# Kernel tuning notes

Measured on AMD Instinct MI355X. Metric: run time of the kernel, lower is better.

The kernel has to match this reference:

```python
import jax, jax.numpy as jnp
import numpy as np

B, L, V, D, C, R = 8, 2048, 32000, 512, 64, 64
NBLK = 2           # n_layers - 1
H = 2 * D          # stem hidden dim
STD = 0.02


def _ln(x, w, b):
    m = x.mean(-1, keepdims=True)
    v = ((x - m) ** 2).mean(-1, keepdims=True)
    return (x - m) / jnp.sqrt(v + 1e-5) * w + b


def setup_inputs() -> dict:
    key = jax.random.key(0)
    ks = jax.random.split(key, 16)
    n = lambda k, shp: jax.random.normal(k, shp, dtype=jnp.float32) * STD
    return {
        "token_ids": jax.random.randint(ks[0], (B, L), 0, V),
        "tok_emb": n(ks[1], (V, D)),
        "pos_emb": n(ks[2], (L, D)),
        "stem_ln_w": jnp.ones((NBLK, D), jnp.float32),
        "stem_ln_b": jnp.zeros((NBLK, D), jnp.float32),
        "stem_w1": n(ks[3], (NBLK, D, H)),
        "stem_b1": jnp.zeros((NBLK, H), jnp.float32),
        "stem_w2": n(ks[4], (NBLK, H, D)),
        "stem_b2": jnp.zeros((NBLK, D), jnp.float32),
        "role_ln_w": jnp.ones((D,), jnp.float32),
        "role_ln_b": jnp.zeros((D,), jnp.float32),
        "Wa": n(ks[5], (D, R)),
        "Wb": n(ks[6], (D, R)),
        "Wc": n(ks[7], (D, R)),
        "class_a": n(ks[8], (C, R)),
        "class_b": n(ks[9], (C, R)),
        "class_c": n(ks[10], (C, R)),
        "query_ln_w": jnp.ones((D,), jnp.float32),
        "query_ln_b": jnp.zeros((D,), jnp.float32),
        "Wq": n(ks[11], (D, C)),
        "bq": jnp.zeros((C,), jnp.float32),
    }


def reference(token_ids, tok_emb, pos_emb, stem_ln_w, stem_ln_b, stem_w1,
              stem_b1, stem_w2, stem_b2, role_ln_w, role_ln_b, Wa, Wb, Wc,
              class_a, class_b, class_c, query_ln_w, query_ln_b, Wq, bq):
    seq_len = token_ids.shape[1]
    x = tok_emb[token_ids] + pos_emb[:seq_len][None, :, :]  # [B,L,D]
    for i in range(NBLK):
        h = _ln(x, stem_ln_w[i], stem_ln_b[i])
        h = jax.nn.gelu(h @ stem_w1[i] + stem_b1[i], approximate=False)
        x = x + h @ stem_w2[i] + stem_b2[i]
    prefix = _ln(x[:, :-1], role_ln_w, role_ln_b)  # [B,L-1,D]
    a = jnp.tanh(prefix @ Wa)
    b = jnp.tanh(prefix @ Wb)
    c = jnp.tanh(prefix @ Wc)
    ua = jnp.einsum('blr,cr->blc', a, class_a)  # [B,L-1,C]
    ub = jnp.einsum('blr,cr->blc', b, class_b)
    uc = jnp.einsum('blr,cr->blc', c, class_c)
    # exact ordered-triplet sum  sum_{i<j<k} ua_i * ub_j * uc_k  via exclusive cumsums
    prefA = jnp.cumsum(ua, axis=1) - ua            # sum_{i<j} ua_i
    t = ub * prefA
    prefT = jnp.cumsum(t, axis=1) - t              # sum_{j<k} ub_j * prefA_j
    s = (uc * prefT).sum(axis=1)                   # [B,C]
    Lp = max(seq_len - 1, 1)
    denom = max(Lp * (Lp - 1) * (Lp - 2) / 6.0, 1.0)
    q = _ln(x[:, -1], query_ln_w, query_ln_b)
    return s / denom + q @ Wq + bq
```

## Files before the change

### kernel.cpp

```cpp
#include <hip/hip_runtime.h>

#define NROWS 16384
#define LSEQ  2048
#define NB    8

typedef short v8s __attribute__((ext_vector_type(8)));
typedef float v4f __attribute__((ext_vector_type(4)));

__device__ __forceinline__ unsigned short f2bf(float f) {
    unsigned int u = __float_as_uint(f);
    return (unsigned short)((u + 0x7fffu + ((u >> 16) & 1u)) >> 16);
}
__device__ __forceinline__ float bf2f(unsigned short u) {
    return __uint_as_float(((unsigned int)u) << 16);
}

__device__ __forceinline__ void glds16(const void* g, void* l) {
    __builtin_amdgcn_global_load_lds(
        (__attribute__((address_space(1))) void*)g,
        (__attribute__((address_space(3))) void*)l,
        16, 0, 0);
}

__device__ __forceinline__ float fast_gelu(float v) {
    float z = fabsf(v) * 0.70710678118654752f;
    float t = __builtin_amdgcn_rcpf(1.0f + 0.3275911f * z);
    float poly = t * (0.254829592f + t * (-0.284496736f + t * (1.421413741f +
                 t * (-1.453152027f + t * 1.061405429f))));
    float erfz = 1.0f - poly * __expf(-z * z);
    float er = copysignf(erfz, v);
    return 0.5f * v * (1.0f + er);
}
__device__ __forceinline__ float fast_tanh(float y) {
    float e = __expf(2.0f * y);
    return (e - 1.0f) * __builtin_amdgcn_rcpf(e + 1.0f);
}

__device__ __forceinline__ long swizzled_row(int b, int wave) {
    int T = (b & 7) + (((b >> 3) & 15) << 3);
    int chunk = b >> 7;
    return (long)T * 128 + chunk * 4 + wave;
}

__global__ __launch_bounds__(256) void setup_kernel(
        const int* __restrict__ ids,
        const float* __restrict__ tok, const float* __restrict__ pos,
        const float* __restrict__ g0, const float* __restrict__ b0,
        const float* __restrict__ rolew, const float* __restrict__ roleb,
        const float* __restrict__ b1all,
        unsigned short* __restrict__ x, float* __restrict__ rowstat0,
        const float* __restrict__ w1, const float* __restrict__ w2,
        const float* __restrict__ wa, const float* __restrict__ wb, const float* __restrict__ wc,
        const float* __restrict__ ca, const float* __restrict__ cb, const float* __restrict__ cc,
        unsigned short* __restrict__ w1T, unsigned short* __restrict__ w2T,
        unsigned short* __restrict__ wabcT, unsigned short* __restrict__ clsb,
        float* __restrict__ c1buf, float* __restrict__ c2buf,
        float* __restrict__ c1a, float* __restrict__ c2a) {
    int blk = blockIdx.x;
    int t = threadIdx.x;
    if (blk < 4096) {
        int wave = t >> 6, lane = t & 63;
        long row = swizzled_row(blk, wave);
        int l = (int)(row & (LSEQ - 1));
        int id = ids[row];
        int d = lane * 8;
        float4 t0 = *(const float4*)(tok + (size_t)id * 512 + d);
        float4 t1 = *(const float4*)(tok + (size_t)id * 512 + d + 4);
        float4 p0 = *(const float4*)(pos + (size_t)l * 512 + d);
        float4 p1 = *(const float4*)(pos + (size_t)l * 512 + d + 4);
        float a[8] = {t0.x + p0.x, t0.y + p0.y, t0.z + p0.z, t0.w + p0.w,
                      t1.x + p1.x, t1.y + p1.y, t1.z + p1.z, t1.w + p1.w};
        unsigned int xp[4];
        #pragma unroll
        for (int i = 0; i < 4; ++i)
            xp[i] = (unsigned int)f2bf(a[2 * i]) | ((unsigned int)f2bf(a[2 * i + 1]) << 16);
        *(uint4*)(x + row * 512 + d) = *(uint4*)xp;
        float s = 0.f, s2 = 0.f;
        #pragma unroll
        for (int i = 0; i < 8; ++i) { s += a[i]; s2 += a[i] * a[i]; }
        #pragma unroll
        for (int o = 32; o > 0; o >>= 1) { s += __shfl_down(s, o); s2 += __shfl_down(s2, o); }
        if (lane == 0) {
            rowstat0[row * 2] = s;
            rowstat0[row * 2 + 1] = s2;
        }
    } else if (blk < 6240) {
        int id = blk - 4096;
        int tx = t & 31, ty = t >> 5;
        const float* in; unsigned short* out; int R, C, bx, by, ldo;
        const float* gfold = nullptr;
        if (id < 1024) {
            int l = id >> 9, r = id & 511;
            in = w1 + l * 524288; out = w1T + l * 524288;
            R = 512; C = 1024; bx = r & 31; by = r >> 5; ldo = 512;
            gfold = g0 + l * 512;
        } else if (id < 2048) {
            int l = (id - 1024) >> 9, r = (id - 1024) & 511;
            in = w2 + l * 524288; out = w2T + l * 524288;
            R = 1024; C = 512; bx = r & 15; by = r >> 4; ldo = 1024;
        } else {
            int g = (id - 2048) >> 5, r = (id - 2048) & 31;
            in = (g == 0) ? wa : (g == 1) ? wb : wc;
            out = wabcT + g * 32768;
            R = 512; C = 64; bx = r & 1; by = r >> 1; ldo = 512;
            gfold = rolew;
        }
        __shared__ unsigned short tile[32][33];
        int c0 = bx * 32, r0 = by * 32;
        for (int i = ty; i < 32; i += 8) {
            int r = r0 + i, c = c0 + tx;
            float v = (r < R && c < C) ? in[(size_t)r * C + c] : 0.f;
            if (gfold && r < R) v *= gfold[r];
            tile[i][tx] = f2bf(v);
        }
        __syncthreads();
        for (int i = ty; i < 32; i += 8) {
            int c = c0 + i, r = r0 + tx;
            if (r < R && c < C) out[(size_t)c * ldo + r] = tile[tx][i];
        }
    } else if (blk < 6243) {
        int g = blk - 6240;
        const float* src = (g == 0) ? ca : (g == 1) ? cb : cc;
        unsigned short* dst = clsb + g * 4096;
        for (int i = t; i < 4096; i += 256) dst[i] = f2bf(src[i]);
    } else if (blk < 6251) {
        int c = blk - 6243;
        int l = c >> 2, nb = c & 3;
        int n = nb * 256 + t;
        const float* W = w1 + l * 524288;
        const float* g = g0 + l * 512;
        const float* b = b0 + l * 512;
        float a1 = 0.f, a2 = 0.f;
        for (int k = 0; k < 512; ++k) {
            float w = W[(size_t)k * 1024 + n];
            a1 += g[k] * w;
            a2 += b[k] * w;
        }
        c1buf[l * 1024 + n] = a1;
        c2buf[l * 1024 + n] = a2 + b1all[l * 1024 + n];
    } else {
        if (t < 192) {
            int gi = t >> 6, r = t & 63;
            const float* W = (gi == 0) ? wa : (gi == 1) ? wb : wc;
            float a1 = 0.f, a2 = 0.f;
            for (int k = 0; k < 512; ++k) {
                float w = W[(size_t)k * 64 + r];
                a1 += rolew[k] * w;
                a2 += roleb[k] * w;
            }
            c1a[t] = a1;
            c2a[t] = a2;
        }
    }
}

template <int SM>
__global__ __launch_bounds__(512, 1) void gemm_w1(
        const unsigned short* __restrict__ A,
        const unsigned short* __restrict__ BT,
        const float* __restrict__ c1, const float* __restrict__ c2,
        const float* __restrict__ stats,
        unsigned short* __restrict__ Cout) {
    constexpr int BN = 256, NFC = 4, FCH = 2, NLB = 2, BH = 128;
    constexpr int lda = 512, ldb = 512, ldc = 1024, K = 512;
    __shared__ unsigned short Ab[2][2][128 * 64] __attribute__((aligned(16)));
    __shared__ unsigned short Bb[2][2][BH * 64] __attribute__((aligned(16)));
    const int t = threadIdx.x;
    const int lane = t & 63, w = t >> 6;
    const int quad = lane >> 4, l16 = lane & 15;
    const int wmh = w >> 2;
    const int wn  = w & 3;
    const int bhalf = wn >> 1, bbase = (wn & 1) * (BN / 4);
    const long tileM = (long)blockIdx.x * 256;
    const long tileN = (long)blockIdx.y * BN;

    const int rl = lane >> 3;
    const int cl = ((lane & 7) ^ rl) * 8;

    const unsigned short* pa[2][2];
    #pragma unroll
    for (int h = 0; h < 2; ++h)
        #pragma unroll
        for (int q = 0; q < 2; ++q)
            pa[h][q] = A + (tileM + h * 128 + w * 16 + q * 8 + rl) * (size_t)lda + cl;
    const unsigned short* pb[2][2];
    #pragma unroll
    for (int h = 0; h < 2; ++h)
        #pragma unroll
        for (int q = 0; q < 2; ++q)
            pb[h][q] = BT + (tileN + h * BH + w * 16 + q * 8 + rl) * (size_t)ldb + cl;
    int kA = 0, kB = 0;

    auto stageA = [&](int buf, int h) {
        glds16(pa[h][0] + kA, &Ab[buf][h][(w * 2 + 0) * 512]);
        glds16(pa[h][1] + kA, &Ab[buf][h][(w * 2 + 1) * 512]);
    };
    auto stageB = [&](int buf, int h) {
        glds16(pb[h][0] + kB, &Bb[buf][h][(w * 2 + 0) * 512]);
        glds16(pb[h][1] + kB, &Bb[buf][h][(w * 2 + 1) * 512]);
    };

    const int xl = l16 & 7;
    const int ak0 = l16 * 64 + (((quad    ) ^ xl) * 8);
    const int ak1 = l16 * 64 + (((quad + 4) ^ xl) * 8);

    stageA(0, 0); stageA(0, 1); kA = 64;
    stageB(0, 0); stageB(0, 1); kB = 64;
    stageB(1, 0); stageB(1, 1); kB = 128;

    v4f acc[8][NFC] = {};
    const int nt = K >> 6;

    asm volatile("s_waitcnt vmcnt(%0)" :: "i"(2 * NLB) : "memory");
    __builtin_amdgcn_s_barrier();

    for (int tt = 0; tt < nt; ++tt) {
        const int bi = tt & 1;
        const unsigned short* Ah = &Ab[bi][wmh][0];
        const unsigned short* Bh = &Bb[bi][bhalf][bbase * 64];
        v8s af[4][2], bf[NFC][2];

        #pragma unroll
        for (int fr = 0; fr < 4; ++fr) {
            af[fr][0] = *(const v8s*)(Ah + fr * 1024 + ak0);
            af[fr][1] = *(const v8s*)(Ah + fr * 1024 + ak1);
        }
        #pragma unroll
        for (int fc = 0; fc < FCH; ++fc) {
            bf[fc][0] = *(const v8s*)(Bh + fc * 1024 + ak0);
            bf[fc][1] = *(const v8s*)(Bh + fc * 1024 + ak1);
        }
        if (tt + 1 < nt) stageA(bi ^ 1, 0);
        __builtin_amdgcn_s_barrier();
        asm volatile("s_waitcnt lgkmcnt(0)" ::: "memory");
        __builtin_amdgcn_s_setprio(1);
        #pragma unroll
        for (int fr = 0; fr < 4; ++fr)
            #pragma unroll
            for (int fc = 0; fc < FCH; ++fc) {
                acc[fr][fc] = __builtin_amdgcn_mfma_f32_16x16x32_bf16(bf[fc][0], af[fr][0], acc[fr][fc], 0, 0, 0);
                acc[fr][fc] = __builtin_amdgcn_mfma_f32_16x16x32_bf16(bf[fc][1], af[fr][1], acc[fr][fc], 0, 0, 0);
            }
        __builtin_amdgcn_s_setprio(0);
        __builtin_amdgcn_s_barrier();

        #pragma unroll
        for (int fc = FCH; fc < NFC; ++fc) {
            bf[fc][0] = *(const v8s*)(Bh + fc * 1024 + ak0);
            bf[fc][1] = *(const v8s*)(Bh + fc * 1024 + ak1);
        }
        if (tt + 1 < nt) stageA(bi ^ 1, 1);
        kA += 64;
        __builtin_amdgcn_s_barrier();
        asm volatile("s_waitcnt lgkmcnt(0)" ::: "memory");
        __builtin_amdgcn_s_setprio(1);
        #pragma unroll
        for (int fr = 0; fr < 4; ++fr)
            #pragma unroll
            for (int fc = FCH; fc < NFC; ++fc) {
                acc[fr][fc] = __builtin_amdgcn_mfma_f32_16x16x32_bf16(bf[fc][0], af[fr][0], acc[fr][fc], 0, 0, 0);
                acc[fr][fc] = __builtin_amdgcn_mfma_f32_16x16x32_bf16(bf[fc][1], af[fr][1], acc[fr][fc], 0, 0, 0);
            }
        __builtin_amdgcn_s_setprio(0);
        __builtin_amdgcn_s_barrier();

        #pragma unroll
        for (int fr = 0; fr < 4; ++fr) {
            af[fr][0] = *(const v8s*)(Ah + (fr + 4) * 1024 + ak0);
            af[fr][1] = *(const v8s*)(Ah + (fr + 4) * 1024 + ak1);
        }
        if (tt + 2 < nt) stageB(bi, 0);
        __builtin_amdgcn_s_barrier();
        asm volatile("s_waitcnt lgkmcnt(0)" ::: "memory");
        __builtin_amdgcn_s_setprio(1);
        #pragma unroll
        for (int fr = 0; fr < 4; ++fr)
            #pragma unroll
            for (int fc = 0; fc < FCH; ++fc) {
                acc[fr + 4][fc] = __builtin_amdgcn_mfma_f32_16x16x32_bf16(bf[fc][0], af[fr][0], acc[fr + 4][fc], 0, 0, 0);
                acc[fr + 4][fc] = __builtin_amdgcn_mfma_f32_16x16x32_bf16(bf[fc][1], af[fr][1], acc[fr + 4][fc], 0, 0, 0);
            }
        __builtin_amdgcn_s_setprio(0);
        __builtin_amdgcn_s_barrier();

        if (tt + 2 < nt) stageB(bi, 1);
        kB += 64;
        if (tt + 2 < nt)
            asm volatile("s_waitcnt vmcnt(%0)" :: "i"(2 * NLB) : "memory");
        else if (tt + 1 < nt)
            asm volatile("s_waitcnt vmcnt(0)" ::: "memory");
        __builtin_amdgcn_s_barrier();
        __builtin_amdgcn_s_setprio(1);
        #pragma unroll
        for (int fr = 0; fr < 4; ++fr)
            #pragma unroll
            for (int fc = FCH; fc < NFC; ++fc) {
                acc[fr + 4][fc] = __builtin_amdgcn_mfma_f32_16x16x32_bf16(bf[fc][0], af[fr][0], acc[fr + 4][fc], 0, 0, 0);
                acc[fr + 4][fc] = __builtin_amdgcn_mfma_f32_16x16x32_bf16(bf[fc][1], af[fr][1], acc[fr + 4][fc], 0, 0, 0);
            }
        __builtin_amdgcn_s_setprio(0);
        __builtin_amdgcn_s_barrier();
    }

    #pragma unroll
    for (int fr = 0; fr < 8; ++fr) {
        long m = tileM + wmh * 128 + fr * 16 + l16;
        float s1, s2;
        if (SM == 0) {
            float2 st = *(const float2*)&stats[m * 2];
            s1 = st.x; s2 = st.y;
        } else {
            float4 q0 = *(const float4*)&stats[m * 8];
            float4 q1 = *(const float4*)&stats[m * 8 + 4];
            s1 = q0.x + q0.z + q1.x + q1.z;
            s2 = q0.y + q0.w + q1.y + q1.w;
        }
        float mu = s1 * (1.0f / 512.0f);
        float rinv = 1.0f / sqrtf(s2 * (1.0f / 512.0f) - mu * mu + 1e-5f);
        float rmu = rinv * mu;
        #pragma unroll
        for (int fc = 0; fc < NFC; ++fc) {
            long n0 = tileN + wn * (BN / 4) + fc * 16 + quad * 4;
            float4 c14 = *(const float4*)&c1[n0];
            float4 c24 = *(const float4*)&c2[n0];
            const float* c1p = (const float*)&c14;
            const float* c2p = (const float*)&c24;
            unsigned short pk[4];
            #pragma unroll
            for (int r = 0; r < 4; ++r)
                pk[r] = f2bf(fast_gelu(rinv * acc[fr][fc][r] - rmu * c1p[r] + c2p[r]));
            *(ushort4*)&Cout[m * ldc + n0] = *(ushort4*)pk;
        }
    }
}

__global__ __launch_bounds__(512, 1) void gemm_w2(
        const unsigned short* __restrict__ A,
        const unsigned short* __restrict__ BT,
        const float* __restrict__ bias,
        unsigned short* __restrict__ x,
        float* __restrict__ rowpart) {
    constexpr int BN = 128, NFC = 2, FCH = 1, NLB = 1, BH = 64;
    constexpr int lda = 1024, ldb = 1024, K = 1024;
    __shared__ unsigned short Ab[2][2][128 * 64] __attribute__((aligned(16)));
    __shared__ unsigned short Bb[2][2][BH * 64] __attribute__((aligned(16)));
    const int t = threadIdx.x;
    const int lane = t & 63, w = t >> 6;
    const int quad = lane >> 4, l16 = lane & 15;
    const int wmh = w >> 2;
    const int wn  = w & 3;
    const int bhalf = wn >> 1, bbase = (wn & 1) * (BN / 4);
    const long tileM = (long)blockIdx.x * 256;
    const int yb = blockIdx.y;
    const long tileN = (long)yb * BN;

    const int rl = lane >> 3;
    const int cl = ((lane & 7) ^ rl) * 8;

    const unsigned short* pa[2][2];
    #pragma unroll
    for (int h = 0; h < 2; ++h)
        #pragma unroll
        for (int q = 0; q < 2; ++q)
            pa[h][q] = A + (tileM + h * 128 + w * 16 + q * 8 + rl) * (size_t)lda + cl;
    const unsigned short* pb[2];
    #pragma unroll
    for (int h = 0; h < 2; ++h)
        pb[h] = BT + (tileN + h * BH + w * 8 + rl) * (size_t)ldb + cl;
    int kA = 0, kB = 0;

    auto stageA = [&](int buf, int h) {
        glds16(pa[h][0] + kA, &Ab[buf][h][(w * 2 + 0) * 512]);
        glds16(pa[h][1] + kA, &Ab[buf][h][(w * 2 + 1) * 512]);
    };
    auto stageB = [&](int buf, int h) {
        glds16(pb[h] + kB, &Bb[buf][h][w * 512]);
    };

    const int xl = l16 & 7;
    const int ak0 = l16 * 64 + (((quad    ) ^ xl) * 8);
    const int ak1 = l16 * 64 + (((quad + 4) ^ xl) * 8);

    stageA(0, 0); stageA(0, 1); kA = 64;
    stageB(0, 0); stageB(0, 1); kB = 64;
    stageB(1, 0); stageB(1, 1); kB = 128;

    v4f acc[8][NFC] = {};
    const int nt = K >> 6;

    asm volatile("s_waitcnt vmcnt(%0)" :: "i"(2 * NLB) : "memory");
    __builtin_amdgcn_s_barrier();

    for (int tt = 0; tt < nt; ++tt) {
        const int bi = tt & 1;
        const unsigned short* Ah = &Ab[bi][wmh][0];
        const unsigned short* Bh = &Bb[bi][bhalf][bbase * 64];
        v8s af[4][2], bf[NFC][2];

        #pragma unroll
        for (int fr = 0; fr < 4; ++fr) {
            af[fr][0] = *(const v8s*)(Ah + fr * 1024 + ak0);
            af[fr][1] = *(const v8s*)(Ah + fr * 1024 + ak1);
        }
        #pragma unroll
        for (int fc = 0; fc < FCH; ++fc) {
            bf[fc][0] = *(const v8s*)(Bh + fc * 1024 + ak0);
            bf[fc][1] = *(const v8s*)(Bh + fc * 1024 + ak1);
        }
        if (tt + 1 < nt) stageA(bi ^ 1, 0);
        __builtin_amdgcn_s_barrier();
        asm volatile("s_waitcnt lgkmcnt(0)" ::: "memory");
        __builtin_amdgcn_s_setprio(1);
        #pragma unroll
        for (int fr = 0; fr < 4; ++fr)
            #pragma unroll
            for (int fc = 0; fc < FCH; ++fc) {
                acc[fr][fc] = __builtin_amdgcn_mfma_f32_16x16x32_bf16(bf[fc][0], af[fr][0], acc[fr][fc], 0, 0, 0);
                acc[fr][fc] = __builtin_amdgcn_mfma_f32_16x16x32_bf16(bf[fc][1], af[fr][1], acc[fr][fc], 0, 0, 0);
            }
        __builtin_amdgcn_s_setprio(0);
        __builtin_amdgcn_s_barrier();

        #pragma unroll
        for (int fc = FCH; fc < NFC; ++fc) {
            bf[fc][0] = *(const v8s*)(Bh + fc * 1024 + ak0);
            bf[fc][1] = *(const v8s*)(Bh + fc * 1024 + ak1);
        }
        if (tt + 1 < nt) stageA(bi ^ 1, 1);
        kA += 64;
        __builtin_amdgcn_s_barrier();
        asm volatile("s_waitcnt lgkmcnt(0)" ::: "memory");
        __builtin_amdgcn_s_setprio(1);
        #pragma unroll
        for (int fr = 0; fr < 4; ++fr)
            #pragma unroll
            for (int fc = FCH; fc < NFC; ++fc) {
                acc[fr][fc] = __builtin_amdgcn_mfma_f32_16x16x32_bf16(bf[fc][0], af[fr][0], acc[fr][fc], 0, 0, 0);
                acc[fr][fc] = __builtin_amdgcn_mfma_f32_16x16x32_bf16(bf[fc][1], af[fr][1], acc[fr][fc], 0, 0, 0);
            }
        __builtin_amdgcn_s_setprio(0);
        __builtin_amdgcn_s_barrier();

        #pragma unroll
        for (int fr = 0; fr < 4; ++fr) {
            af[fr][0] = *(const v8s*)(Ah + (fr + 4) * 1024 + ak0);
            af[fr][1] = *(const v8s*)(Ah + (fr + 4) * 1024 + ak1);
        }
        if (tt + 2 < nt) stageB(bi, 0);
        __builtin_amdgcn_s_barrier();
        asm volatile("s_waitcnt lgkmcnt(0)" ::: "memory");
        __builtin_amdgcn_s_setprio(1);
        #pragma unroll
        for (int fr = 0; fr < 4; ++fr)
            #pragma unroll
            for (int fc = 0; fc < FCH; ++fc) {
                acc[fr + 4][fc] = __builtin_amdgcn_mfma_f32_16x16x32_bf16(bf[fc][0], af[fr][0], acc[fr + 4][fc], 0, 0, 0);
                acc[fr + 4][fc] = __builtin_amdgcn_mfma_f32_16x16x32_bf16(bf[fc][1], af[fr][1], acc[fr + 4][fc], 0, 0, 0);
            }
        __builtin_amdgcn_s_setprio(0);
        __builtin_amdgcn_s_barrier();

        if (tt + 2 < nt) stageB(bi, 1);
        kB += 64;
        if (tt + 2 < nt)
            asm volatile("s_waitcnt vmcnt(%0)" :: "i"(2 * NLB) : "memory");
        else if (tt + 1 < nt)
            asm volatile("s_waitcnt vmcnt(0)" ::: "memory");
        __builtin_amdgcn_s_barrier();
        __builtin_amdgcn_s_setprio(1);
        #pragma unroll
        for (int fr = 0; fr < 4; ++fr)
            #pragma unroll
            for (int fc = FCH; fc < NFC; ++fc) {
                acc[fr + 4][fc] = __builtin_amdgcn_mfma_f32_16x16x32_bf16(bf[fc][0], af[fr][0], acc[fr + 4][fc], 0, 0, 0);
                acc[fr + 4][fc] = __builtin_amdgcn_mfma_f32_16x16x32_bf16(bf[fc][1], af[fr][1], acc[fr + 4][fc], 0, 0, 0);
            }
        __builtin_amdgcn_s_setprio(0);
        __builtin_amdgcn_s_barrier();
    }

    float p1[8], p2[8];
    #pragma unroll
    for (int fr = 0; fr < 8; ++fr) { p1[fr] = 0.f; p2[fr] = 0.f; }
    #pragma unroll
    for (int fr = 0; fr < 8; ++fr) {
        long m = tileM + wmh * 128 + fr * 16 + l16;
        #pragma unroll
        for (int fc = 0; fc < NFC; ++fc) {
            long n0 = tileN + wn * (BN / 4) + fc * 16 + quad * 4;
            float4 bi4 = *(const float4*)&bias[n0 - tileN + yb * BN];
            const float* bip = (const float*)&bi4;
            ushort4 xr4 = *(const ushort4*)&x[m * 512 + n0];
            const unsigned short* xp = (const unsigned short*)&xr4;
            unsigned short pk[4];
            #pragma unroll
            for (int r = 0; r < 4; ++r) {
                float v = acc[fr][fc][r] + bip[r] + bf2f(xp[r]);
                p1[fr] += v; p2[fr] += v * v;
                pk[r] = f2bf(v);
            }
            *(ushort4*)&x[m * 512 + n0] = *(ushort4*)pk;
        }
    }
    #pragma unroll
    for (int fr = 0; fr < 8; ++fr) {
        p1[fr] += __shfl_xor(p1[fr], 16); p1[fr] += __shfl_xor(p1[fr], 32);
        p2[fr] += __shfl_xor(p2[fr], 16); p2[fr] += __shfl_xor(p2[fr], 32);
    }
    float* red = (float*)&Ab[0][0][0];
    if (quad == 0) {
        #pragma unroll
        for (int fr = 0; fr < 8; ++fr) {
            int r = wmh * 128 + fr * 16 + l16;
            red[r * 4 + wn] = p1[fr];
            red[1024 + r * 4 + wn] = p2[fr];
        }
    }
    __syncthreads();
    if (t < 256) {
        int r = t;
        float s1 = red[r * 4] + red[r * 4 + 1] + red[r * 4 + 2] + red[r * 4 + 3];
        float s2 = red[1024 + r * 4] + red[1024 + r * 4 + 1] + red[1024 + r * 4 + 2] + red[1024 + r * 4 + 3];
        long m = tileM + r;
        rowpart[m * 8 + yb * 2]     = s1;
        rowpart[m * 8 + yb * 2 + 1] = s2;
    }
}

__global__ __launch_bounds__(256) void tanh_class_kernel(
        const unsigned short* __restrict__ A,
        const unsigned short* __restrict__ WT,
        const unsigned short* __restrict__ cls,
        const float* __restrict__ rowpart,
        const float* __restrict__ c1a, const float* __restrict__ c2a,
        unsigned short* __restrict__ uu) {
    __shared__ unsigned short As[128][40] __attribute__((aligned(16)));
    __shared__ unsigned short Bs[64][40] __attribute__((aligned(16)));
    __shared__ unsigned short P[128 * 72] __attribute__((aligned(16)));
    const int t = threadIdx.x;
    const int lane = t & 63, wave = t >> 6;
    const int quad = lane >> 4, l16 = lane & 15;
    const int wm = (wave >> 1) * 64, wn = (wave & 1) * 32;
    const long tileM = (long)blockIdx.x * 128;
    const int g = blockIdx.y;
    const int arow = t >> 2, acol = (t & 3) * 8;

    const unsigned short* BT = WT + g * 32768;
    v8s cf[2][2];
    #pragma unroll
    for (int ks = 0; ks < 2; ++ks)
        #pragma unroll
        for (int j = 0; j < 2; ++j)
            cf[ks][j] = *(const v8s*)&cls[g * 4096 + (wn + j * 16 + l16) * 64 + ks * 32 + quad * 8];

    const unsigned short* gA0 = A + (tileM + arow) * 512 + acol;
    const unsigned short* gA1 = gA0 + 64 * 512;
    const unsigned short* gB0 = BT + arow * 512 + acol;

    v4f acc[4][2] = {};
    uint4 a0, a1, b0;
    a0 = *(const uint4*)gA0; a1 = *(const uint4*)gA1; gA0 += 32; gA1 += 32;
    b0 = *(const uint4*)gB0; gB0 += 32;
    *(uint4*)&As[arow][acol] = a0;
    *(uint4*)&As[arow + 64][acol] = a1;
    *(uint4*)&Bs[arow][acol] = b0;

    for (int kk = 0; kk < 16; ++kk) {
        __syncthreads();
        const bool more = kk < 15;
        if (more) {
            a0 = *(const uint4*)gA0; a1 = *(const uint4*)gA1; gA0 += 32; gA1 += 32;
            b0 = *(const uint4*)gB0; gB0 += 32;
        }
        v8s af[4], bfr[2];
        #pragma unroll
        for (int i = 0; i < 4; ++i) af[i] = *(const v8s*)&As[wm + i * 16 + l16][quad * 8];
        #pragma unroll
        for (int j = 0; j < 2; ++j) bfr[j] = *(const v8s*)&Bs[wn + j * 16 + l16][quad * 8];
        #pragma unroll
        for (int i = 0; i < 4; ++i)
            #pragma unroll
            for (int j = 0; j < 2; ++j)
                acc[i][j] = __builtin_amdgcn_mfma_f32_16x16x32_bf16(bfr[j], af[i], acc[i][j], 0, 0, 0);
        __syncthreads();
        if (more) {
            *(uint4*)&As[arow][acol] = a0;
            *(uint4*)&As[arow + 64][acol] = a1;
            *(uint4*)&Bs[arow][acol] = b0;
        }
    }

    #pragma unroll
    for (int i = 0; i < 4; ++i) {
        int m = wm + i * 16 + l16;
        long gm = tileM + m;
        float4 q0 = *(const float4*)&rowpart[gm * 8];
        float4 q1 = *(const float4*)&rowpart[gm * 8 + 4];
        float s1 = q0.x + q0.z + q1.x + q1.z;
        float s2 = q0.y + q0.w + q1.y + q1.w;
        float mu = s1 * (1.0f / 512.0f);
        float rinv = 1.0f / sqrtf(s2 * (1.0f / 512.0f) - mu * mu + 1e-5f);
        float rmu = rinv * mu;
        #pragma unroll
        for (int j = 0; j < 2; ++j) {
            int n0 = wn + j * 16 + quad * 4;
            float4 c14 = *(const float4*)&c1a[g * 64 + n0];
            float4 c24 = *(const float4*)&c2a[g * 64 + n0];
            const float* c1p = (const float*)&c14;
            const float* c2p = (const float*)&c24;
            unsigned short pk[4];
            #pragma unroll
            for (int r = 0; r < 4; ++r)
                pk[r] = f2bf(fast_tanh(rinv * acc[i][j][r] - rmu * c1p[r] + c2p[r]));
            *(ushort4*)&P[m * 72 + n0] = *(ushort4*)pk;
        }
    }
    __syncthreads();

    v4f acc2[4][2] = {};
    #pragma unroll
    for (int ks = 0; ks < 2; ++ks) {
        v8s paf[4];
        #pragma unroll
        for (int i = 0; i < 4; ++i)
            paf[i] = *(const v8s*)&P[(wm + i * 16 + l16) * 72 + ks * 32 + quad * 8];
        #pragma unroll
        for (int i = 0; i < 4; ++i)
            #pragma unroll
            for (int j = 0; j < 2; ++j)
                acc2[i][j] = __builtin_amdgcn_mfma_f32_16x16x32_bf16(cf[ks][j], paf[i], acc2[i][j], 0, 0, 0);
    }

    #pragma unroll
    for (int i = 0; i < 4; ++i) {
        long m = tileM + wm + i * 16 + l16;
        #pragma unroll
        for (int j = 0; j < 2; ++j) {
            int c0 = wn + j * 16 + quad * 4;
            unsigned short pk[4];
            #pragma unroll
            for (int r = 0; r < 4; ++r) pk[r] = f2bf(acc2[i][j][r]);
            *(ushort4*)&uu[m * 192 + g * 64 + c0] = *(ushort4*)pk;
        }
    }
}

__global__ __launch_bounds__(64) void scan_part_kernel(const unsigned short* __restrict__ u,
                                                       float* __restrict__ part) {
    int b = blockIdx.x, seg = blockIdx.y;
    int c = threadIdx.x;
    int l0 = seg * 32;
    int l1 = l0 + 32; if (l1 > 2047) l1 = 2047;
    float sA = 0.f, sB = 0.f, sC = 0.f, T = 0.f, M = 0.f, U = 0.f;
    const unsigned short* base = u + ((size_t)b * LSEQ + l0) * 192 + c;
    for (int l = l0; l < l1; ++l) {
        float ua = bf2f(base[0]), ub = bf2f(base[64]), uc = bf2f(base[128]);
        base += 192;
        U += uc * T;
        M += uc * sB;
        T += ub * sA;
        sA += ua; sB += ub; sC += uc;
    }
    float* p = part + ((size_t)(b * 64 + seg)) * 384 + c;
    p[0] = sA; p[64] = sB; p[128] = sC; p[192] = T; p[256] = M; p[320] = U;
}

__global__ __launch_bounds__(64) void combine_final_kernel(const float* __restrict__ part,
        const unsigned short* __restrict__ x,
        const float* __restrict__ qw, const float* __restrict__ qb,
        const float* __restrict__ Wq, const float* __restrict__ bq,
        float* __restrict__ out, float inv_denom) {
    int b = blockIdx.x;
    int c = threadIdx.x;
    const float* p = part + (size_t)b * 64 * 384 + c;
    float A = p[0], B = p[64], Tt = p[192], Mt = p[256], Ut = p[320];
    for (int seg = 1; seg < 64; ++seg) {
        const float* q2 = p + seg * 384;
        float a2 = q2[0], b2 = q2[64], c2 = q2[128], t2 = q2[192], m2 = q2[256], u2 = q2[320];
        float Un = Ut + u2 + c2 * Tt + A * m2;
        float Tn = Tt + t2 + A * b2;
        float Mn = Mt + m2 + B * c2;
        A += a2; B += b2;
        Ut = Un; Tt = Tn; Mt = Mn;
    }
    __shared__ float q[512];
    __shared__ float mv[2];
    const unsigned short* xr = x + ((size_t)b * LSEQ + (LSEQ - 1)) * 512;
    float s1 = 0.f, s2 = 0.f;
    for (int i = c; i < 512; i += 64) { float v = bf2f(xr[i]); q[i] = v; s1 += v; s2 += v * v; }
    #pragma unroll
    for (int o = 32; o > 0; o >>= 1) { s1 += __shfl_down(s1, o); s2 += __shfl_down(s2, o); }
    if (c == 0) {
        float m = s1 * (1.0f / 512.0f);
        float var = s2 * (1.0f / 512.0f) - m * m;
        mv[0] = m; mv[1] = 1.0f / sqrtf(var + 1e-5f);
    }
    __syncthreads();
    float m = mv[0], r = mv[1];
    for (int i = c; i < 512; i += 64) q[i] = (q[i] - m) * r * qw[i] + qb[i];
    __syncthreads();
    float acc = 0.f;
    for (int d = 0; d < 512; ++d) acc += q[d] * Wq[d * 64 + c];
    out[b * 64 + c] = Ut * inv_denom + acc + bq[c];
}

extern "C" void kernel_launch(void* const* d_in, const int* in_sizes, int n_in,
                              void* d_out, int out_size, void* d_ws, size_t ws_size,
                              hipStream_t stream) {
    const int*   token_ids   = (const int*)d_in[0];
    const float* tok_emb     = (const float*)d_in[1];
    const float* pos_emb     = (const float*)d_in[2];
    const float* stem_ln_w   = (const float*)d_in[3];
    const float* stem_ln_b   = (const float*)d_in[4];
    const float* stem_w1     = (const float*)d_in[5];
    const float* stem_b1     = (const float*)d_in[6];
    const float* stem_w2     = (const float*)d_in[7];
    const float* stem_b2     = (const float*)d_in[8];
    const float* role_ln_w   = (const float*)d_in[9];
    const float* role_ln_b   = (const float*)d_in[10];
    const float* Wa          = (const float*)d_in[11];
    const float* Wb          = (const float*)d_in[12];
    const float* Wc          = (const float*)d_in[13];
    const float* class_a     = (const float*)d_in[14];
    const float* class_b     = (const float*)d_in[15];
    const float* class_c     = (const float*)d_in[16];
    const float* query_ln_w  = (const float*)d_in[17];
    const float* query_ln_b  = (const float*)d_in[18];
    const float* Wq          = (const float*)d_in[19];
    const float* bq          = (const float*)d_in[20];
    float* out = (float*)d_out;

    char* wsb = (char*)d_ws;
    unsigned short* x    = (unsigned short*)(wsb);
    unsigned short* Hb   = (unsigned short*)(wsb + 16777216);
    unsigned short* uu   = (unsigned short*)(wsb + 50331648);
    float* part          = (float*)(wsb + 56623104);
    unsigned short* w1T  = (unsigned short*)(wsb + 57409536);
    unsigned short* w2T  = (unsigned short*)(wsb + 59506688);
    unsigned short* wabcT= (unsigned short*)(wsb + 61603840);
    unsigned short* clsb = (unsigned short*)(wsb + 61800448);
    float* rowstat0      = (float*)(wsb + 61825024);
    float* rowpart1      = (float*)(wsb + 61956096);
    float* rowpart2      = (float*)(wsb + 62480384);
    float* c1buf         = (float*)(wsb + 63004672);
    float* c2buf         = (float*)(wsb + 63012864);
    float* c1a           = (float*)(wsb + 63021056);
    float* c2a           = (float*)(wsb + 63021824);

    setup_kernel<<<6252, 256, 0, stream>>>(token_ids, tok_emb, pos_emb,
        stem_ln_w, stem_ln_b, role_ln_w, role_ln_b, stem_b1,
        x, rowstat0,
        stem_w1, stem_w2, Wa, Wb, Wc, class_a, class_b, class_c,
        w1T, w2T, wabcT, clsb, c1buf, c2buf, c1a, c2a);

    gemm_w1<0><<<dim3(64, 4), 512, 0, stream>>>(
        x, w1T, c1buf, c2buf, rowstat0, Hb);
    gemm_w2<<<dim3(64, 4), 512, 0, stream>>>(
        Hb, w2T, stem_b2, x, rowpart1);
    gemm_w1<1><<<dim3(64, 4), 512, 0, stream>>>(
        x, w1T + 524288, c1buf + 1024, c2buf + 1024, rowpart1, Hb);
    gemm_w2<<<dim3(64, 4), 512, 0, stream>>>(
        Hb, w2T + 524288, stem_b2 + 512, x, rowpart2);

    tanh_class_kernel<<<dim3(128, 3), 256, 0, stream>>>(x, wabcT, clsb,
                                                        rowpart2, c1a, c2a, uu);

    scan_part_kernel<<<dim3(NB, 64), 64, 0, stream>>>(uu, part);

    float inv_denom = (float)(6.0 / (2047.0 * 2046.0 * 2045.0));
    combine_final_kernel<<<NB, 64, 0, stream>>>(part, x, query_ln_w, query_ln_b,
                                                Wq, bq, out, inv_denom);
}
```

Before: 346.6 us.

## Fuse tanh/class projection with segment scan and parallelize setup reductions

Merges the tanh-projection/class GEMM kernel with the segment scan kernel. Each 64-row block now computes all three role groups, keeps the projected scores in LDS and scans them directly, so the bf16 uu buffer no longer goes through global memory and one launch disappears. The setup-time weight folds (c1/c2 for the stem and role LN) are split across more blocks with a k-split and an LDS reduction instead of 512-long serial loops. The changes also simplify a bias index in gemm_w2, and the fused kernel trades grid parallelism (256 blocks, with one wave doing the scan) for less memory traffic.

Result: faster. 326.6 us (-5.7%).

```diff
diff --git a/kernel.cpp b/kernel.cpp
--- a/kernel.cpp
+++ b/kernel.cpp
@@ -123,33 +123,52 @@
         const float* src = (g == 0) ? ca : (g == 1) ? cb : cc;
         unsigned short* dst = clsb + g * 4096;
         for (int i = t; i < 4096; i += 256) dst[i] = f2bf(src[i]);
-    } else if (blk < 6251) {
-        int c = blk - 6243;
-        int l = c >> 2, nb = c & 3;
-        int n = nb * 256 + t;
+    } else if (blk < 6307) {
+        int idx = blk - 6243;
+        int l = idx >> 5, nch = idx & 31;
+        int n = nch * 32 + (t & 31);
+        int kq = t >> 5;
         const float* W = w1 + l * 524288;
         const float* g = g0 + l * 512;
         const float* b = b0 + l * 512;
         float a1 = 0.f, a2 = 0.f;
-        for (int k = 0; k < 512; ++k) {
+        for (int k = kq * 64; k < kq * 64 + 64; ++k) {
             float w = W[(size_t)k * 1024 + n];
             a1 += g[k] * w;
             a2 += b[k] * w;
         }
-        c1buf[l * 1024 + n] = a1;
-        c2buf[l * 1024 + n] = a2 + b1all[l * 1024 + n];
+        __shared__ float red1[8][32], red2[8][32];
+        red1[kq][t & 31] = a1;
+        red2[kq][t & 31] = a2;
+        __syncthreads();
+        if (t < 32) {
+            float s1 = 0.f, s2 = 0.f;
+            #pragma unroll
+            for (int q = 0; q < 8; ++q) { s1 += red1[q][t]; s2 += red2[q][t]; }
+            int nn = nch * 32 + t;
+            c1buf[l * 1024 + nn] = s1;
+            c2buf[l * 1024 + nn] = s2 + b1all[l * 1024 + nn];
+        }
     } else {
-        if (t < 192) {
-            int gi = t >> 6, r = t & 63;
-            const float* W = (gi == 0) ? wa : (gi == 1) ? wb : wc;
-            float a1 = 0.f, a2 = 0.f;
-            for (int k = 0; k < 512; ++k) {
-                float w = W[(size_t)k * 64 + r];
-                a1 += rolew[k] * w;
-                a2 += roleb[k] * w;
-            }
-            c1a[t] = a1;
-            c2a[t] = a2;
+        int gi = blk - 6307;
+        const float* W = (gi == 0) ? wa : (gi == 1) ? wb : wc;
+        int n = t & 63, kq = t >> 6;
+        float a1 = 0.f, a2 = 0.f;
+        for (int k = kq * 128; k < kq * 128 + 128; ++k) {
+            float w = W[(size_t)k * 64 + n];
+            a1 += rolew[k] * w;
+            a2 += roleb[k] * w;
+        }
+        __shared__ float red1[4][64], red2[4][64];
+        red1[kq][n] = a1;
+        red2[kq][n] = a2;
+        __syncthreads();
+        if (t < 64) {
+            float s1 = 0.f, s2 = 0.f;
+            #pragma unroll
+            for (int q = 0; q < 4; ++q) { s1 += red1[q][t]; s2 += red2[q][t]; }
+            c1a[gi * 64 + t] = s1;
+            c2a[gi * 64 + t] = s2;
         }
     }
 }
@@ -488,7 +507,7 @@
         #pragma unroll
         for (int fc = 0; fc < NFC; ++fc) {
             long n0 = tileN + wn * (BN / 4) + fc * 16 + quad * 4;
-            float4 bi4 = *(const float4*)&bias[n0 - tileN + yb * BN];
+            float4 bi4 = *(const float4*)&bias[n0];
             const float* bip = (const float*)&bi4;
             ushort4 xr4 = *(const ushort4*)&x[m * 512 + n0];
             const unsigned short* xp = (const unsigned short*)&xr4;
@@ -527,72 +546,63 @@
     }
 }
 
-__global__ __launch_bounds__(256) void tanh_class_kernel(
+__global__ __launch_bounds__(256) void tanh_scan_kernel(
         const unsigned short* __restrict__ A,
         const unsigned short* __restrict__ WT,
         const unsigned short* __restrict__ cls,
         const float* __restrict__ rowpart,
         const float* __restrict__ c1a, const float* __restrict__ c2a,
-        unsigned short* __restrict__ uu) {
-    __shared__ unsigned short As[128][40] __attribute__((aligned(16)));
-    __shared__ unsigned short Bs[64][40] __attribute__((aligned(16)));
-    __shared__ unsigned short P[128 * 72] __attribute__((aligned(16)));
+        float* __restrict__ part) {
+    __shared__ unsigned short As[64][40] __attribute__((aligned(16)));
+    __shared__ unsigned short Bs[3][64][40] __attribute__((aligned(16)));
+    __shared__ unsigned short P[3][64 * 72] __attribute__((aligned(16)));
+    __shared__ unsigned short U[64][200] __attribute__((aligned(16)));
     const int t = threadIdx.x;
-    const int lane = t & 63, wave = t >> 6;
+    const int lane = t & 63, w = t >> 6;
     const int quad = lane >> 4, l16 = lane & 15;
-    const int wm = (wave >> 1) * 64, wn = (wave & 1) * 32;
-    const long tileM = (long)blockIdx.x * 128;
-    const int g = blockIdx.y;
+    const long tileM = (long)blockIdx.x * 64;
     const int arow = t >> 2, acol = (t & 3) * 8;
-
-    const unsigned short* BT = WT + g * 32768;
-    v8s cf[2][2];
-    #pragma unroll
-    for (int ks = 0; ks < 2; ++ks)
-        #pragma unroll
-        for (int j = 0; j < 2; ++j)
-            cf[ks][j] = *(const v8s*)&cls[g * 4096 + (wn + j * 16 + l16) * 64 + ks * 32 + quad * 8];
-
-    const unsigned short* gA0 = A + (tileM + arow) * 512 + acol;
-    const unsigned short* gA1 = gA0 + 64 * 512;
-    const unsigned short* gB0 = BT + arow * 512 + acol;
-
-    v4f acc[4][2] = {};
-    uint4 a0, a1, b0;
-    a0 = *(const uint4*)gA0; a1 = *(const uint4*)gA1; gA0 += 32; gA1 += 32;
-    b0 = *(const uint4*)gB0; gB0 += 32;
+    const int m = w * 16 + l16;
+
+    const unsigned short* gA = A + (tileM + arow) * 512 + acol;
+    const unsigned short* gB[3];
+    #pragma unroll
+    for (int g = 0; g < 3; ++g) gB[g] = WT + g * 32768 + arow * 512 + acol;
+
+    v4f acc[3][4] = {};
+    uint4 a0, b0[3];
+    a0 = *(const uint4*)gA; gA += 32;
+    #pragma unroll
+    for (int g = 0; g < 3; ++g) { b0[g] = *(const uint4*)gB[g]; gB[g] += 32; }
     *(uint4*)&As[arow][acol] = a0;
-    *(uint4*)&As[arow + 64][acol] = a1;
-    *(uint4*)&Bs[arow][acol] = b0;
+    #pragma unroll
+    for (int g = 0; g < 3; ++g) *(uint4*)&Bs[g][arow][acol] = b0[g];
 
     for (int kk = 0; kk < 16; ++kk) {
         __syncthreads();
         const bool more = kk < 15;
         if (more) {
-            a0 = *(const uint4*)gA0; a1 = *(const uint4*)gA1; gA0 += 32; gA1 += 32;
-            b0 = *(const uint4*)gB0; gB0 += 32;
-        }
-        v8s af[4], bfr[2];
-        #pragma unroll
-        for (int i = 0; i < 4; ++i) af[i] = *(const v8s*)&As[wm + i * 16 + l16][quad * 8];
-        #pragma unroll
-        for (int j = 0; j < 2; ++j) bfr[j] = *(const v8s*)&Bs[wn + j * 16 + l16][quad * 8];
-        #pragma unroll
-        for (int i = 0; i < 4; ++i)
-            #pragma unroll
-            for (int j = 0; j < 2; ++j)
-                acc[i][j] = __builtin_amdgcn_mfma_f32_16x16x32_bf16(bfr[j], af[i], acc[i][j], 0, 0, 0);
+            a0 = *(const uint4*)gA; gA += 32;
+            #pragma unroll
+            for (int g = 0; g < 3; ++g) { b0[g] = *(const uint4*)gB[g]; gB[g] += 32; }
+        }
+        v8s af = *(const v8s*)&As[m][quad * 8];
+        #pragma unroll
+        for (int g = 0; g < 3; ++g)
+            #pragma unroll
+            for (int fc = 0; fc < 4; ++fc) {
+                v8s bfr = *(const v8s*)&Bs[g][fc * 16 + l16][quad * 8];
+                acc[g][fc] = __builtin_amdgcn_mfma_f32_16x16x32_bf16(bfr, af, acc[g][fc], 0, 0, 0);
+            }
         __syncthreads();
         if (more) {
             *(uint4*)&As[arow][acol] = a0;
-            *(uint4*)&As[arow + 64][acol] = a1;
-            *(uint4*)&Bs[arow][acol] = b0;
-        }
-    }
-
-    #pragma unroll
-    for (int i = 0; i < 4; ++i) {
-        int m = wm + i * 16 + l16;
+            #pragma unroll
+            for (int g = 0; g < 3; ++g) *(uint4*)&Bs[g][arow][acol] = b0[g];
+        }
+    }
+
+    {
         long gm = tileM + m;
         float4 q0 = *(const float4*)&rowpart[gm * 8];
         float4 q1 = *(const float4*)&rowpart[gm * 8 + 4];
@@ -602,67 +612,64 @@
         float rinv = 1.0f / sqrtf(s2 * (1.0f / 512.0f) - mu * mu + 1e-5f);
         float rmu = rinv * mu;
         #pragma unroll
-        for (int j = 0; j < 2; ++j) {
-            int n0 = wn + j * 16 + quad * 4;
-            float4 c14 = *(const float4*)&c1a[g * 64 + n0];
-            float4 c24 = *(const float4*)&c2a[g * 64 + n0];
-            const float* c1p = (const float*)&c14;
-            const float* c2p = (const float*)&c24;
+        for (int g = 0; g < 3; ++g)
+            #pragma unroll
+            for (int fc = 0; fc < 4; ++fc) {
+                int n0 = fc * 16 + quad * 4;
+                float4 c14 = *(const float4*)&c1a[g * 64 + n0];
+                float4 c24 = *(const float4*)&c2a[g * 64 + n0];
+                const float* c1p = (const float*)&c14;
+                const float* c2p = (const float*)&c24;
+                unsigned short pk[4];
+                #pragma unroll
+                for (int r = 0; r < 4; ++r)
+                    pk[r] = f2bf(fast_tanh(rinv * acc[g][fc][r] - rmu * c1p[r] + c2p[r]));
+                *(ushort4*)&P[g][m * 72 + n0] = *(ushort4*)pk;
+            }
+    }
+    __syncthreads();
+
+    #pragma unroll
+    for (int g = 0; g < 3; ++g) {
+        v4f acc2[4] = {};
+        #pragma unroll
+        for (int ks = 0; ks < 2; ++ks) {
+            v8s paf = *(const v8s*)&P[g][m * 72 + ks * 32 + quad * 8];
+            #pragma unroll
+            for (int jc = 0; jc < 4; ++jc) {
+                v8s cf = *(const v8s*)&cls[g * 4096 + (jc * 16 + l16) * 64 + ks * 32 + quad * 8];
+                acc2[jc] = __builtin_amdgcn_mfma_f32_16x16x32_bf16(cf, paf, acc2[jc], 0, 0, 0);
+            }
+        }
+        #pragma unroll
+        for (int jc = 0; jc < 4; ++jc) {
+            int c0 = jc * 16 + quad * 4;
             unsigned short pk[4];
             #pragma unroll
-            for (int r = 0; r < 4; ++r)
-                pk[r] = f2bf(fast_tanh(rinv * acc[i][j][r] - rmu * c1p[r] + c2p[r]));
-            *(ushort4*)&P[m * 72 + n0] = *(ushort4*)pk;
+            for (int r = 0; r < 4; ++r) pk[r] = f2bf(acc2[jc][r]);
+            *(ushort4*)&U[m][g * 64 + c0] = *(ushort4*)pk;
         }
     }
     __syncthreads();
 
-    v4f acc2[4][2] = {};
-    #pragma unroll
-    for (int ks = 0; ks < 2; ++ks) {
-        v8s paf[4];
-        #pragma unroll
-        for (int i = 0; i < 4; ++i)
-            paf[i] = *(const v8s*)&P[(wm + i * 16 + l16) * 72 + ks * 32 + quad * 8];
-        #pragma unroll
-        for (int i = 0; i < 4; ++i)
-            #pragma unroll
-            for (int j = 0; j < 2; ++j)
-                acc2[i][j] = __builtin_amdgcn_mfma_f32_16x16x32_bf16(cf[ks][j], paf[i], acc2[i][j], 0, 0, 0);
-    }
-
-    #pragma unroll
-    for (int i = 0; i < 4; ++i) {
-        long m = tileM + wm + i * 16 + l16;
-        #pragma unroll
-        for (int j = 0; j < 2; ++j) {
-            int c0 = wn + j * 16 + quad * 4;
-            unsigned short pk[4];
-            #pragma unroll
-            for (int r = 0; r < 4; ++r) pk[r] = f2bf(acc2[i][j][r]);
-            *(ushort4*)&uu[m * 192 + g * 64 + c0] = *(ushort4*)pk;
-        }
-    }
-}
-
-__global__ __launch_bounds__(64) void scan_part_kernel(const unsigned short* __restrict__ u,
-                                                       float* __restrict__ part) {
-    int b = blockIdx.x, seg = blockIdx.y;
-    int c = threadIdx.x;
-    int l0 = seg * 32;
-    int l1 = l0 + 32; if (l1 > 2047) l1 = 2047;
-    float sA = 0.f, sB = 0.f, sC = 0.f, T = 0.f, M = 0.f, U = 0.f;
-    const unsigned short* base = u + ((size_t)b * LSEQ + l0) * 192 + c;
-    for (int l = l0; l < l1; ++l) {
-        float ua = bf2f(base[0]), ub = bf2f(base[64]), uc = bf2f(base[128]);
-        base += 192;
-        U += uc * T;
-        M += uc * sB;
-        T += ub * sA;
-        sA += ua; sB += ub; sC += uc;
-    }
-    float* p = part + ((size_t)(b * 64 + seg)) * 384 + c;
-    p[0] = sA; p[64] = sB; p[128] = sC; p[192] = T; p[256] = M; p[320] = U;
+    if (t < 64) {
+        int c = t;
+        int nl = (((int)(tileM & (LSEQ - 1))) == LSEQ - 64) ? 63 : 64;
+        float sA = 0.f, sB = 0.f, sC = 0.f, T = 0.f, M = 0.f, Uu = 0.f;
+        for (int l = 0; l < nl; ++l) {
+            float ua = bf2f(U[l][c]);
+            float ub = bf2f(U[l][64 + c]);
+            float uc = bf2f(U[l][128 + c]);
+            Uu += uc * T;
+            M += uc * sB;
+            T += ub * sA;
+            sA += ua; sB += ub; sC += uc;
+        }
+        int b = (int)(tileM >> 11);
+        int seg = (int)(tileM >> 6) & 31;
+        float* p = part + ((size_t)(b * 32 + seg)) * 384 + c;
+        p[0] = sA; p[64] = sB; p[128] = sC; p[192] = T; p[256] = M; p[320] = Uu;
+    }
 }
 
 __global__ __launch_bounds__(64) void combine_final_kernel(const float* __restrict__ part,
@@ -672,9 +679,9 @@
         float* __restrict__ out, float inv_denom) {
     int b = blockIdx.x;
     int c = threadIdx.x;
-    const float* p = part + (size_t)b * 64 * 384 + c;
+    const float* p = part + (size_t)b * 32 * 384 + c;
     float A = p[0], B = p[64], Tt = p[192], Mt = p[256], Ut = p[320];
-    for (int seg = 1; seg < 64; ++seg) {
+    for (int seg = 1; seg < 32; ++seg) {
         const float* q2 = p + seg * 384;
         float a2 = q2[0], b2 = q2[64], c2 = q2[128], t2 = q2[192], m2 = q2[256], u2 = q2[320];
         float Un = Ut + u2 + c2 * Tt + A * m2;
@@ -733,21 +740,20 @@
     char* wsb = (char*)d_ws;
     unsigned short* x    = (unsigned short*)(wsb);
     unsigned short* Hb   = (unsigned short*)(wsb + 16777216);
-    unsigned short* uu   = (unsigned short*)(wsb + 50331648);
-    float* part          = (float*)(wsb + 56623104);
-    unsigned short* w1T  = (unsigned short*)(wsb + 57409536);
-    unsigned short* w2T  = (unsigned short*)(wsb + 59506688);
-    unsigned short* wabcT= (unsigned short*)(wsb + 61603840);
-    unsigned short* clsb = (unsigned short*)(wsb + 61800448);
-    float* rowstat0      = (float*)(wsb + 61825024);
-    float* rowpart1      = (float*)(wsb + 61956096);
-    float* rowpart2      = (float*)(wsb + 62480384);
-    float* c1buf         = (float*)(wsb + 63004672);
-    float* c2buf         = (float*)(wsb + 63012864);
-    float* c1a           = (float*)(wsb + 63021056);
-    float* c2a           = (float*)(wsb + 63021824);
-
-    setup_kernel<<<6252, 256, 0, stream>>>(token_ids, tok_emb, pos_emb,
+    float* part          = (float*)(wsb + 50331648);
+    unsigned short* w1T  = (unsigned short*)(wsb + 51118080);
+    unsigned short* w2T  = (unsigned short*)(wsb + 53215232);
+    unsigned short* wabcT= (unsigned short*)(wsb + 55312384);
+    unsigned short* clsb = (unsigned short*)(wsb + 55508992);
+    float* rowstat0      = (float*)(wsb + 55533568);
+    float* rowpart1      = (float*)(wsb + 55664640);
+    float* rowpart2      = (float*)(wsb + 56188928);
+    float* c1buf         = (float*)(wsb + 56713216);
+    float* c2buf         = (float*)(wsb + 56721408);
+    float* c1a           = (float*)(wsb + 56729600);
+    float* c2a           = (float*)(wsb + 56730368);
+
+    setup_kernel<<<6310, 256, 0, stream>>>(token_ids, tok_emb, pos_emb,
         stem_ln_w, stem_ln_b, role_ln_w, role_ln_b, stem_b1,
         x, rowstat0,
         stem_w1, stem_w2, Wa, Wb, Wc, class_a, class_b, class_c,
@@ -762,10 +768,8 @@
     gemm_w2<<<dim3(64, 4), 512, 0, stream>>>(
         Hb, w2T + 524288, stem_b2 + 512, x, rowpart2);
 
-    tanh_class_kernel<<<dim3(128, 3), 256, 0, stream>>>(x, wabcT, clsb,
-                                                        rowpart2, c1a, c2a, uu);
-
-    scan_part_kernel<<<dim3(NB, 64), 64, 0, stream>>>(uu, part);
+    tanh_scan_kernel<<<256, 256, 0, stream>>>(x, wabcT, clsb,
+                                              rowpart2, c1a, c2a, part);
 
     float inv_denom = (float)(6.0 / (2047.0 * 2046.0 * 2045.0));
     combine_final_kernel<<<NB, 64, 0, stream>>>(part, x, query_ln_w, query_ln_b,
```
